# Performance work log

Measured on AMD Instinct MI355X. Metric: run time of the kernel, lower is better.

The kernel has to match this reference:

```python
import jax, jax.numpy as jnp
import numpy as np

B, S, D = 128, 144, 1024  # batch, grid tokens (12x12), d_model
GRID = 12


def _relative_position(grid_size):
    # Reconstructs get_grids_pos for a grid_size x grid_size grid of unit cells
    # (x_min = cell col/row index, x_max = x_min + 1), standard grid-feature layout.
    x = jnp.arange(grid_size, dtype=jnp.float32)
    px_min = jnp.repeat(x, grid_size)          # (S,) varies slowly (rows)
    py_min = jnp.tile(x, grid_size)            # (S,) varies fast (cols)
    px_max = px_min + 1.0
    py_max = py_min + 1.0
    cx = (px_min + px_max) * 0.5
    cy = (py_min + py_max) * 0.5
    w = px_max - px_min + 1.0                  # == 2 everywhere
    h = py_max - py_min + 1.0
    eps = 1e-10
    dx = jnp.log(jnp.maximum(jnp.abs((cx[:, None] - cx[None, :]) / w[:, None]), eps))
    dy = jnp.log(jnp.maximum(jnp.abs((cy[:, None] - cy[None, :]) / h[:, None]), eps))
    dw = jnp.log(w[:, None] / w[None, :])
    dh = jnp.log(h[:, None] / h[None, :])
    return jnp.stack([dx, dy, dw, dh], axis=-1)  # (S, S, 4)


def setup_inputs() -> dict:
    key = jax.random.key(0)
    ks = jax.random.split(key, 12)
    std = 0.02
    return {
        "query": jax.random.normal(ks[0], (B, S, D), jnp.float32),
        "key":   jax.random.normal(ks[1], (B, S, D), jnp.float32),
        "value": jax.random.normal(ks[2], (B, S, D), jnp.float32),
        # Linear weights stored as (in, out): y = x @ W + b
        "Wq": jax.random.normal(ks[3], (D, D), jnp.float32) * std,
        "bq": jnp.zeros((D,), jnp.float32),
        "Wk": jax.random.normal(ks[4], (D, D), jnp.float32) * std,
        "bk": jnp.zeros((D,), jnp.float32),
        "Wv": jax.random.normal(ks[5], (D, D), jnp.float32) * std,
        "bv": jnp.zeros((D,), jnp.float32),
        "Wl": jax.random.normal(ks[6], (4, D), jnp.float32) * std,
        "bl": jnp.zeros((D,), jnp.float32),
        "w_g": jax.random.normal(ks[7], (S, D, 1), jnp.float32) * std,
    }


def reference(query, key, value, Wq, bq, Wk, bk, Wv, bv, Wl, bl, w_g):
    d_model = query.shape[-1]
    scale = d_model ** (-0.5)
    act = jax.nn.relu  # get_activation_function() assumed relu; dropout=0 (eval)

    q = act(query @ Wq + bq)   # (B,S,D)
    k = act(key @ Wk + bk)
    v = act(value @ Wv + bv)

    attn = jnp.einsum('bid,bjd->bij', q, k) * scale  # (B,S,S)

    seq = value.shape[1]
    pos = _relative_position(int(round(seq ** 0.5)))  # (S,S,4)
    rel = act(pos @ Wl + bl)                          # (S,S,D)
    # torch.matmul(rela_pos, w_g): row i of the grid uses w_g[i]
    bias = act(jnp.einsum('ijd,id->ij', rel, w_g[..., 0]))  # (S,S)

    attn = jax.nn.softmax(attn + bias[None, :, :], axis=-1)
    return jnp.einsum('bij,bjd->bid', attn, v)
```

## Files before the change

### kernel.cpp

```cpp
#include <hip/hip_runtime.h>
#include <hip/hip_bf16.h>
#include <stdint.h>

#define SS 144
#define DD 1024
#define NB 128
#define SP 160
#define SCALE 0.03125f

typedef __attribute__((ext_vector_type(8))) short short8;
typedef __attribute__((ext_vector_type(4))) float floatx4;
typedef unsigned short u16;

#define MFMA(a, b, c) __builtin_amdgcn_mfma_f32_16x16x32_bf16((a), (b), (c), 0, 0, 0)

__device__ __forceinline__ u16 f2bf(float f) {
    union { float f; unsigned int i; } v; v.f = f;
    unsigned int r = v.i + 0x7fff + ((v.i >> 16) & 1);
    return (u16)(r >> 16);
}
__device__ __forceinline__ short8 pack8(float4 a, float4 b) {
    short8 r;
    r[0] = (short)f2bf(a.x); r[1] = (short)f2bf(a.y);
    r[2] = (short)f2bf(a.z); r[3] = (short)f2bf(a.w);
    r[4] = (short)f2bf(b.x); r[5] = (short)f2bf(b.y);
    r[6] = (short)f2bf(b.z); r[7] = (short)f2bf(b.w);
    return r;
}

__device__ __forceinline__ void gload16(u16* lds, const u16* g) {
    __builtin_amdgcn_global_load_lds(
        (__attribute__((address_space(1))) void*)g,
        (__attribute__((address_space(3))) void*)lds, 16, 0, 0);
}

__global__ __launch_bounds__(256) void convert3_k(
    const float* __restrict__ Xq, const float* __restrict__ Xk,
    const float* __restrict__ Xv,
    u16* __restrict__ Oq, u16* __restrict__ Ok, u16* __restrict__ Ov, int nchunk) {
    int z = blockIdx.y;
    const float* X = z == 0 ? Xq : (z == 1 ? Xk : Xv);
    u16* O = z == 0 ? Oq : (z == 1 ? Ok : Ov);
    for (int c = blockIdx.x * 256 + threadIdx.x; c < nchunk; c += gridDim.x * 256) {
        size_t i = (size_t)c * 8;
        float4 a = *(const float4*)(X + i);
        float4 b = *(const float4*)(X + i + 4);
        *(short8*)(O + i) = pack8(a, b);
    }
}

__global__ void transpose_w_k(const float* __restrict__ Wq, const float* __restrict__ Wk,
                              const float* __restrict__ Wv, u16* __restrict__ WT) {
    __shared__ u16 t[32][33];
    int z = blockIdx.z;
    const float* W = z == 0 ? Wq : (z == 1 ? Wk : Wv);
    u16* O = WT + (size_t)z * DD * DD;
    int bn = blockIdx.x * 32, bk = blockIdx.y * 32;
    int tx = threadIdx.x & 31, ty = threadIdx.x >> 5;
    for (int r = ty; r < 32; r += 8) t[r][tx] = f2bf(W[(size_t)(bk + r) * DD + bn + tx]);
    __syncthreads();
    for (int r = ty; r < 32; r += 8) O[(size_t)(bn + r) * DD + bk + tx] = t[tx][r];
}

__global__ void bias_k(const float* __restrict__ Wl, const float* __restrict__ bl,
                       const float* __restrict__ wg, float* __restrict__ biasb) {
    int ij = blockIdx.x;
    int i = ij / SS, j = ij - i * SS;
    int lane = threadIdx.x;
    int ri = i / 12, ci = i - ri * 12, rj = j / 12, cj = j - rj * 12;
    float dx = logf(fmaxf(fabsf((float)(ri - rj)) * 0.5f, 1e-10f));
    float dy = logf(fmaxf(fabsf((float)(ci - cj)) * 0.5f, 1e-10f));
    float s = 0.f;
    for (int d = lane; d < DD; d += 64) {
        float r = dx * Wl[d] + dy * Wl[DD + d] + bl[d];
        r = fmaxf(r, 0.f);
        s += r * wg[(size_t)i * DD + d];
    }
    #pragma unroll
    for (int m = 32; m > 0; m >>= 1) s += __shfl_xor(s, m);
    if (lane == 0) biasb[ij] = fmaxf(s, 0.f);
}

__global__ __launch_bounds__(256) void proj_k(
    const u16* __restrict__ Xq, const u16* __restrict__ Xk, const u16* __restrict__ Xv,
    const u16* __restrict__ WT,
    const float* __restrict__ bq, const float* __restrict__ bk, const float* __restrict__ bv,
    u16* __restrict__ Oq, u16* __restrict__ Ok, u16* __restrict__ OvT) {
    __shared__ __align__(16) u16 As[128 * 32];
    __shared__ __align__(16) u16 Bs[128 * 32];
    int z = blockIdx.z;
    const u16* Xb = z == 0 ? Xq : (z == 1 ? Xk : Xv);
    const u16* Wt = WT + (size_t)z * DD * DD;
    const float* bias = z == 0 ? bq : (z == 1 ? bk : bv);
    int bm = blockIdx.x, bn = blockIdx.y;
    int tid = threadIdx.x, lane = tid & 63, wv = tid >> 6;
    int wm = wv >> 1, wn = wv & 1;
    int lr = lane & 15, lq = lane >> 4;

    floatx4 zero4 = {0.f, 0.f, 0.f, 0.f};
    floatx4 acc[4][4];
    #pragma unroll
    for (int r = 0; r < 4; r++)
        #pragma unroll
        for (int c = 0; c < 4; c++) acc[r][c] = zero4;

    const u16* Abase = Xb + (size_t)bm * 128 * DD;
    const u16* Bbase = Wt + (size_t)bn * 128 * DD;

    int c0 = tid, c1 = tid + 256;
    const u16* ga0 = Abase + (size_t)(c0 >> 2) * DD + ((c0 & 3) << 3);
    const u16* ga1 = Abase + (size_t)(c1 >> 2) * DD + ((c1 & 3) << 3);
    const u16* gb0 = Bbase + (size_t)(c0 >> 2) * DD + ((c0 & 3) << 3);
    const u16* gb1 = Bbase + (size_t)(c1 >> 2) * DD + ((c1 & 3) << 3);
    u16* la0 = &As[c0 * 8];
    u16* la1 = &As[c1 * 8];
    u16* lb0 = &Bs[c0 * 8];
    u16* lb1 = &Bs[c1 * 8];

    for (int k0 = 0; k0 < DD; k0 += 32) {
        __syncthreads();
        gload16(la0, ga0 + k0);
        gload16(la1, ga1 + k0);
        gload16(lb0, gb0 + k0);
        gload16(lb1, gb1 + k0);
        __syncthreads();
        short8 a[4], b[4];
        #pragma unroll
        for (int r = 0; r < 4; r++)
            a[r] = *(const short8*)&As[(wm * 64 + r * 16 + lr) * 32 + lq * 8];
        #pragma unroll
        for (int c = 0; c < 4; c++)
            b[c] = *(const short8*)&Bs[(wn * 64 + c * 16 + lr) * 32 + lq * 8];
        #pragma unroll
        for (int r = 0; r < 4; r++)
            #pragma unroll
            for (int c = 0; c < 4; c++)
                acc[r][c] = MFMA(a[r], b[c], acc[r][c]);
    }

    int mrow0 = bm * 128 + wm * 64;
    int ncol0 = bn * 128 + wn * 64;
    if (z < 2) {
        u16* O = z == 0 ? Oq : Ok;
        #pragma unroll
        for (int r = 0; r < 4; r++)
            #pragma unroll
            for (int c = 0; c < 4; c++) {
                int col = ncol0 + c * 16 + lr;
                float bb = bias[col];
                #pragma unroll
                for (int i = 0; i < 4; i++) {
                    int row = mrow0 + r * 16 + lq * 4 + i;
                    O[(size_t)row * DD + col] = f2bf(fmaxf(acc[r][c][i] + bb, 0.f));
                }
            }
    } else {
        #pragma unroll
        for (int r = 0; r < 4; r++)
            #pragma unroll
            for (int c = 0; c < 4; c++) {
                int col = ncol0 + c * 16 + lr;
                float bb = bias[col];
                #pragma unroll
                for (int i = 0; i < 4; i++) {
                    int row = mrow0 + r * 16 + lq * 4 + i;
                    int bidx = row / SS;
                    int srow = row - bidx * SS;
                    OvT[((size_t)bidx * DD + col) * SP + srow] =
                        f2bf(fmaxf(acc[r][c][i] + bb, 0.f));
                }
            }
    }
}

__global__ __launch_bounds__(256) void attn_pv_k(
    const u16* __restrict__ q, const u16* __restrict__ k,
    const u16* __restrict__ vT, const float* __restrict__ biasb,
    float* __restrict__ out) {
    __shared__ float Sst[16][148];
    __shared__ __align__(16) u16 Pst[16][168];
    int it = blockIdx.x, b = blockIdx.y;
    int i0 = it * 16;
    int tid = threadIdx.x, lane = tid & 63, wv = tid >> 6;
    int lr = lane & 15, lq = lane >> 4;
    const u16* qs = q + ((size_t)b * SS + i0) * DD;
    const u16* ks = k + (size_t)b * SS * DD;

    floatx4 zero4 = {0.f, 0.f, 0.f, 0.f};
    floatx4 acc[3] = {zero4, zero4, zero4};
    int nt = (wv == 0) ? 3 : 2;

    for (int d0 = 0; d0 < DD; d0 += 32) {
        short8 a = *(const short8*)&qs[(size_t)lr * DD + d0 + lq * 8];
        #pragma unroll
        for (int m = 0; m < 3; m++) {
            if (m < nt) {
                int t = wv + m * 4;
                short8 bb = *(const short8*)&ks[(size_t)(t * 16 + lr) * DD + d0 + lq * 8];
                acc[m] = MFMA(a, bb, acc[m]);
            }
        }
    }
    for (int m = 0; m < nt; m++) {
        int t = wv + m * 4;
        #pragma unroll
        for (int i = 0; i < 4; i++) {
            int row = lq * 4 + i, col = t * 16 + lr;
            Sst[row][col] = acc[m][i] * SCALE + biasb[(i0 + row) * SS + col];
        }
    }
    __syncthreads();

    {
        int g = tid >> 4, j = tid & 15;
        float mx = -1e30f;
        for (int c = j; c < SS; c += 16) mx = fmaxf(mx, Sst[g][c]);
        #pragma unroll
        for (int m = 1; m < 16; m <<= 1) mx = fmaxf(mx, __shfl_xor(mx, m));
        float sm = 0.f;
        float ev[9];
        int t = 0;
        for (int c = j; c < SS; c += 16, t++) { float e = expf(Sst[g][c] - mx); ev[t] = e; sm += e; }
        #pragma unroll
        for (int m = 1; m < 16; m <<= 1) sm += __shfl_xor(sm, m);
        float inv = 1.f / sm;
        t = 0;
        for (int c = j; c < SP; c += 16, t++) {
            float val = (c < SS) ? ev[t < 9 ? t : 8] * inv : 0.f;
            Pst[g][c] = f2bf(val);
        }
    }
    __syncthreads();

    const u16* vt = vT + (size_t)b * DD * SP;
    float* ob = out + ((size_t)b * SS + i0) * DD;
    #pragma unroll 4
    for (int m = 0; m < 16; m++) {
        int colb = wv * 256 + m * 16;
        floatx4 pacc = zero4;
        #pragma unroll
        for (int k0 = 0; k0 < SP; k0 += 32) {
            short8 a = *(const short8*)&Pst[lr][k0 + lq * 8];
            short8 bb = *(const short8*)&vt[(size_t)(colb + lr) * SP + k0 + lq * 8];
            pacc = MFMA(a, bb, pacc);
        }
        #pragma unroll
        for (int i = 0; i < 4; i++)
            ob[(size_t)(lq * 4 + i) * DD + colb + lr] = pacc[i];
    }
}

extern "C" void kernel_launch(void* const* d_in, const int* in_sizes, int n_in,
                              void* d_out, int out_size, void* d_ws, size_t ws_size,
                              hipStream_t stream) {
    const float* query = (const float*)d_in[0];
    const float* key_  = (const float*)d_in[1];
    const float* value = (const float*)d_in[2];
    const float* Wq = (const float*)d_in[3];
    const float* bq = (const float*)d_in[4];
    const float* Wk = (const float*)d_in[5];
    const float* bk = (const float*)d_in[6];
    const float* Wv = (const float*)d_in[7];
    const float* bv = (const float*)d_in[8];
    const float* Wl = (const float*)d_in[9];
    const float* bl = (const float*)d_in[10];
    const float* wg = (const float*)d_in[11];

    u16* WT    = (u16*)d_ws;
    u16* Xv    = WT + (size_t)3 * DD * DD;
    u16* q     = Xv + (size_t)NB * SS * DD;
    u16* k     = q  + (size_t)NB * SS * DD;
    u16* vT    = k  + (size_t)NB * SS * DD;
    float* biasb = (float*)(vT + (size_t)NB * DD * SP);

    u16* Xq = (u16*)d_out;
    u16* Xk = Xq + (size_t)NB * SS * DD;

    transpose_w_k<<<dim3(32, 32, 3), 256, 0, stream>>>(Wq, Wk, Wv, WT);
    bias_k<<<dim3(SS * SS), 64, 0, stream>>>(Wl, bl, wg, biasb);

    int nchunk = NB * SS * DD / 8;
    convert3_k<<<dim3(1024, 3), 256, 0, stream>>>(query, key_, value, Xq, Xk, Xv, nchunk);
    proj_k<<<dim3(144, 8, 3), 256, 0, stream>>>(Xq, Xk, Xv, WT, bq, bk, bv, q, k, vT);

    attn_pv_k<<<dim3(9, NB), 256, 0, stream>>>(q, k, vT, biasb, (float*)d_out);
}
```

Measured before the change: 644.6 us.

## Process whole batch per attention block with LDS-staged K and swap projection grid order

The attention kernel now handles all 144 query rows of a batch in one 576-thread block. K tiles are staged through shared memory and reused across the 9 waves, and the softmax is done in registers. The PV stage then reuses each V fragment across all row tiles, so K and V are no longer reloaded from global memory by 9 separate blocks per batch. The projection grid is reordered so consecutive blocks share the same activation row tile. The trade-off is only 128 attention blocks, which lowers occupancy and parallelism, and only 8 of the 9 waves do the PV work.

```diff
diff --git a/kernel.cpp b/kernel.cpp
--- a/kernel.cpp
+++ b/kernel.cpp
@@ -92,7 +92,7 @@
     const u16* Xb = z == 0 ? Xq : (z == 1 ? Xk : Xv);
     const u16* Wt = WT + (size_t)z * DD * DD;
     const float* bias = z == 0 ? bq : (z == 1 ? bk : bv);
-    int bm = blockIdx.x, bn = blockIdx.y;
+    int bn = blockIdx.x, bm = blockIdx.y;
     int tid = threadIdx.x, lane = tid & 63, wv = tid >> 6;
     int wm = wv >> 1, wn = wv & 1;
     int lr = lane & 15, lq = lane >> 4;
@@ -173,80 +173,112 @@
     }
 }
 
-__global__ __launch_bounds__(256) void attn_pv_k(
+__global__ __launch_bounds__(576) void attn_fused_k(
     const u16* __restrict__ q, const u16* __restrict__ k,
     const u16* __restrict__ vT, const float* __restrict__ biasb,
     float* __restrict__ out) {
-    __shared__ float Sst[16][148];
-    __shared__ __align__(16) u16 Pst[16][168];
-    int it = blockIdx.x, b = blockIdx.y;
-    int i0 = it * 16;
+    __shared__ __align__(16) u16 smem[24192];
+    u16* kst = smem;
+    u16* Pst = smem;
+    int b = blockIdx.x;
     int tid = threadIdx.x, lane = tid & 63, wv = tid >> 6;
     int lr = lane & 15, lq = lane >> 4;
-    const u16* qs = q + ((size_t)b * SS + i0) * DD;
+    const u16* qs = q + (size_t)b * SS * DD;
     const u16* ks = k + (size_t)b * SS * DD;
 
-    floatx4 zero4 = {0.f, 0.f, 0.f, 0.f};
-    floatx4 acc[3] = {zero4, zero4, zero4};
-    int nt = (wv == 0) ? 3 : 2;
-
-    for (int d0 = 0; d0 < DD; d0 += 32) {
-        short8 a = *(const short8*)&qs[(size_t)lr * DD + d0 + lq * 8];
-        #pragma unroll
-        for (int m = 0; m < 3; m++) {
-            if (m < nt) {
-                int t = wv + m * 4;
-                short8 bb = *(const short8*)&ks[(size_t)(t * 16 + lr) * DD + d0 + lq * 8];
-                acc[m] = MFMA(a, bb, acc[m]);
+    floatx4 acc[9];
+    #pragma unroll
+    for (int c = 0; c < 9; c++) acc[c] = (floatx4){0.f, 0.f, 0.f, 0.f};
+    int c0 = tid, c1 = tid + 576;
+    int r0 = c0 >> 3, o0 = (c0 & 7) << 3;
+    int r1 = c1 >> 3, o1 = (c1 & 7) << 3;
+    int qrow = wv * 16 + lr;
+    for (int d0 = 0; d0 < DD; d0 += 64) {
+        short8 v0 = *(const short8*)&ks[(size_t)r0 * DD + d0 + o0];
+        short8 v1 = *(const short8*)&ks[(size_t)r1 * DD + d0 + o1];
+        short8 a0 = *(const short8*)&qs[(size_t)qrow * DD + d0 + lq * 8];
+        short8 a1 = *(const short8*)&qs[(size_t)qrow * DD + d0 + 32 + lq * 8];
+        __syncthreads();
+        *(short8*)&kst[r0 * 72 + o0] = v0;
+        *(short8*)&kst[r1 * 72 + o1] = v1;
+        __syncthreads();
+        #pragma unroll
+        for (int ct = 0; ct < 9; ct++) {
+            short8 b0 = *(const short8*)&kst[(ct * 16 + lr) * 72 + lq * 8];
+            acc[ct] = MFMA(a0, b0, acc[ct]);
+        }
+        #pragma unroll
+        for (int ct = 0; ct < 9; ct++) {
+            short8 b1 = *(const short8*)&kst[(ct * 16 + lr) * 72 + 32 + lq * 8];
+            acc[ct] = MFMA(a1, b1, acc[ct]);
+        }
+    }
+    __syncthreads();
+
+    int row0 = wv * 16 + lq * 4;
+    float sv[9][4], mx[4], sm[4];
+    #pragma unroll
+    for (int i = 0; i < 4; i++) mx[i] = -1e30f;
+    #pragma unroll
+    for (int ct = 0; ct < 9; ct++)
+        #pragma unroll
+        for (int i = 0; i < 4; i++) {
+            float s = acc[ct][i] * SCALE + biasb[(row0 + i) * SS + ct * 16 + lr];
+            sv[ct][i] = s;
+            mx[i] = fmaxf(mx[i], s);
+        }
+    #pragma unroll
+    for (int i = 0; i < 4; i++) {
+        #pragma unroll
+        for (int m = 1; m < 16; m <<= 1) mx[i] = fmaxf(mx[i], __shfl_xor(mx[i], m));
+        sm[i] = 0.f;
+    }
+    #pragma unroll
+    for (int ct = 0; ct < 9; ct++)
+        #pragma unroll
+        for (int i = 0; i < 4; i++) {
+            float e = expf(sv[ct][i] - mx[i]);
+            sv[ct][i] = e;
+            sm[i] += e;
+        }
+    #pragma unroll
+    for (int i = 0; i < 4; i++) {
+        #pragma unroll
+        for (int m = 1; m < 16; m <<= 1) sm[i] += __shfl_xor(sm[i], m);
+        sm[i] = 1.f / sm[i];
+    }
+    #pragma unroll
+    for (int ct = 0; ct < 9; ct++)
+        #pragma unroll
+        for (int i = 0; i < 4; i++)
+            Pst[(row0 + i) * 168 + ct * 16 + lr] = f2bf(sv[ct][i] * sm[i]);
+    #pragma unroll
+    for (int i = 0; i < 4; i++)
+        Pst[(row0 + i) * 168 + 144 + lr] = 0;
+    __syncthreads();
+
+    if (wv < 8) {
+        const u16* vt = vT + (size_t)b * DD * SP;
+        float* ob = out + (size_t)b * SS * DD;
+        int colb = wv * 128;
+        for (int ct2 = 0; ct2 < 8; ct2++) {
+            int col = colb + ct2 * 16 + lr;
+            short8 vb[5];
+            #pragma unroll
+            for (int kk = 0; kk < 5; kk++)
+                vb[kk] = *(const short8*)&vt[(size_t)col * SP + kk * 32 + lq * 8];
+            for (int rt = 0; rt < 9; rt++) {
+                floatx4 f = {0.f, 0.f, 0.f, 0.f};
+                #pragma unroll
+                for (int kk = 0; kk < 5; kk++) {
+                    short8 a = *(const short8*)&Pst[(rt * 16 + lr) * 168 + kk * 32 + lq * 8];
+                    f = MFMA(a, vb[kk], f);
+                }
+                #pragma unroll
+                for (int i = 0; i < 4; i++)
+                    ob[(size_t)(rt * 16 + lq * 4 + i) * DD + col] = f[i];
             }
         }
-    }
-    for (int m = 0; m < nt; m++) {
-        int t = wv + m * 4;
-        #pragma unroll
-        for (int i = 0; i < 4; i++) {
-            int row = lq * 4 + i, col = t * 16 + lr;
-            Sst[row][col] = acc[m][i] * SCALE + biasb[(i0 + row) * SS + col];
-        }
-    }
-    __syncthreads();
-
-    {
-        int g = tid >> 4, j = tid & 15;
-        float mx = -1e30f;
-        for (int c = j; c < SS; c += 16) mx = fmaxf(mx, Sst[g][c]);
-        #pragma unroll
-        for (int m = 1; m < 16; m <<= 1) mx = fmaxf(mx, __shfl_xor(mx, m));
-        float sm = 0.f;
-        float ev[9];
-        int t = 0;
-        for (int c = j; c < SS; c += 16, t++) { float e = expf(Sst[g][c] - mx); ev[t] = e; sm += e; }
-        #pragma unroll
-        for (int m = 1; m < 16; m <<= 1) sm += __shfl_xor(sm, m);
-        float inv = 1.f / sm;
-        t = 0;
-        for (int c = j; c < SP; c += 16, t++) {
-            float val = (c < SS) ? ev[t < 9 ? t : 8] * inv : 0.f;
-            Pst[g][c] = f2bf(val);
-        }
-    }
-    __syncthreads();
-
-    const u16* vt = vT + (size_t)b * DD * SP;
-    float* ob = out + ((size_t)b * SS + i0) * DD;
-    #pragma unroll 4
-    for (int m = 0; m < 16; m++) {
-        int colb = wv * 256 + m * 16;
-        floatx4 pacc = zero4;
-        #pragma unroll
-        for (int k0 = 0; k0 < SP; k0 += 32) {
-            short8 a = *(const short8*)&Pst[lr][k0 + lq * 8];
-            short8 bb = *(const short8*)&vt[(size_t)(colb + lr) * SP + k0 + lq * 8];
-            pacc = MFMA(a, bb, pacc);
-        }
-        #pragma unroll
-        for (int i = 0; i < 4; i++)
-            ob[(size_t)(lq * 4 + i) * DD + colb + lr] = pacc[i];
     }
 }
 
@@ -281,7 +313,7 @@
 
     int nchunk = NB * SS * DD / 8;
     convert3_k<<<dim3(1024, 3), 256, 0, stream>>>(query, key_, value, Xq, Xk, Xv, nchunk);
-    proj_k<<<dim3(144, 8, 3), 256, 0, stream>>>(Xq, Xk, Xv, WT, bq, bk, bv, q, k, vT);
-
-    attn_pv_k<<<dim3(9, NB), 256, 0, stream>>>(q, k, vT, biasb, (float*)d_out);
-}
+    proj_k<<<dim3(8, 144, 3), 256, 0, stream>>>(Xq, Xk, Xv, WT, bq, bk, bv, q, k, vT);
+
+    attn_fused_k<<<dim3(NB), 576, 0, stream>>>(q, k, vT, biasb, (float*)d_out);
+}
```

Result: slower. 663.8 us (+3.0%).
